# Optimization experiments

Measured on AMD Instinct MI355X. Metric: run time of the kernel, lower is better.

Reference implementation:

```python
import jax, jax.numpy as jnp
import numpy as np

B, D, U = 8192, 2048, 2048  # batch rows, input dim, units
NB_FACTOR = 3
MASK_DENSITY = 1.0 / 16.0  # butterfly-like sparse factor density


def _glorot_uniform(key, shape):
    fan_in, fan_out = shape[0], shape[-1]
    limit = np.sqrt(6.0 / (fan_in + fan_out)).astype(np.float32)
    return jax.random.uniform(key, shape, jnp.float32, -limit, limit)


def setup_inputs() -> dict:
    key = jax.random.key(0)
    kx, km0, km1, km2, kk0, kk1, kk2, ks = jax.random.split(key, 8)
    x = jax.random.normal(kx, (B, D), jnp.float32)
    # Fixed sparsity patterns (constants, like K.constant sparsity_masks)
    m0 = (jax.random.uniform(km0, (D, U)) < MASK_DENSITY).astype(jnp.float32)
    m1 = (jax.random.uniform(km1, (U, U)) < MASK_DENSITY).astype(jnp.float32)
    m2 = (jax.random.uniform(km2, (U, U)) < MASK_DENSITY).astype(jnp.float32)
    k0 = _glorot_uniform(kk0, (D, U))
    k1 = _glorot_uniform(kk1, (U, U))
    k2 = _glorot_uniform(kk2, (U, U))
    scaling = _glorot_uniform(ks, (1,))  # scaler weight, shape (1,)
    bias = jnp.zeros((U,), jnp.float32)
    return {"x": x, "k0": k0, "k1": k1, "k2": k2,
            "m0": m0, "m1": m1, "m2": m2,
            "scaling": scaling, "bias": bias}


def reference(x, k0, k1, k2, m0, m1, m2, scaling, bias):
    # output = activation(scaling * (x @ (k0*m0) @ (k1*m1) @ (k2*m2)) + bias)
    out = x @ (k0 * m0)          # [B, U]
    out = out @ (k1 * m1)        # [B, U]
    out = out @ (k2 * m2)        # [B, U]
    out = scaling * out + bias   # scale then channels-last bias add
    return jax.nn.relu(out)
```

## Files before the change

kernel.cpp:

```cpp
#include <hip/hip_runtime.h>
#include <hip/hip_bf16.h>


typedef __attribute__((ext_vector_type(8))) short  short8;
typedef __attribute__((ext_vector_type(8))) ushort ushort8v;
typedef __attribute__((ext_vector_type(4))) float  f32x4;

#define KD 2048
#define ND 2048

__device__ __forceinline__ ushort f2b(float f) {
    union { float f; unsigned u; } v; v.f = f;
    unsigned r = v.u + 0x7fffu + ((v.u >> 16) & 1u);
    return (ushort)(r >> 16);
}

__device__ __forceinline__ void gload16(const ushort* g, ushort* l) {
    __builtin_amdgcn_global_load_lds(
        (const __attribute__((address_space(1))) void*)g,
        (__attribute__((address_space(3))) void*)l, 16, 0, 0);
}

__global__ __launch_bounds__(256)
void convx(const float* __restrict__ x, ushort* __restrict__ xb)
{
    const size_t i = (size_t)blockIdx.x * 256 + threadIdx.x;
    const float4* src = reinterpret_cast<const float4*>(x) + i * 2;
    const float4 f0 = src[0], f1 = src[1];
    ushort8v u;
    u[0]=f2b(f0.x); u[1]=f2b(f0.y); u[2]=f2b(f0.z); u[3]=f2b(f0.w);
    u[4]=f2b(f1.x); u[5]=f2b(f1.y); u[6]=f2b(f1.z); u[7]=f2b(f1.w);
    reinterpret_cast<ushort8v*>(xb)[i] = u;
}

__global__ __launch_bounds__(256)
void convT3(const float* __restrict__ k0w, const float* __restrict__ k1w,
            const float* __restrict__ k2w, const float* __restrict__ m0w,
            const float* __restrict__ m1w, const float* __restrict__ m2w,
            ushort* __restrict__ wbT)
{
    const int z = blockIdx.z;
    const float* kw = z == 0 ? k0w : (z == 1 ? k1w : k2w);
    const float* mw = z == 0 ? m0w : (z == 1 ? m1w : m2w);
    ushort* o = wbT + (size_t)z * KD * ND;

    __shared__ ushort t[32][36];
    const int tid = threadIdx.x;
    const int bk = blockIdx.x * 32, bn = blockIdx.y * 32;
    {
        const int r = tid >> 3, c = (tid & 7) * 4;
        const size_t g = (size_t)(bk + r) * ND + bn + c;
        const float4 kv = *reinterpret_cast<const float4*>(kw + g);
        const float4 mv = *reinterpret_cast<const float4*>(mw + g);
        t[r][c + 0] = f2b(kv.x * mv.x);
        t[r][c + 1] = f2b(kv.y * mv.y);
        t[r][c + 2] = f2b(kv.z * mv.z);
        t[r][c + 3] = f2b(kv.w * mv.w);
    }
    __syncthreads();
    {
        const int n = tid >> 3, kq = (tid & 7) * 4;
        ushort4 ov;
        ov.x = t[kq + 0][n]; ov.y = t[kq + 1][n];
        ov.z = t[kq + 2][n]; ov.w = t[kq + 3][n];
        *reinterpret_cast<ushort4*>(&o[(size_t)(bn + n) * KD + bk + kq]) = ov;
    }
}

template<int EPI>
__global__ __launch_bounds__(512, 2)
void gemm256(const ushort* __restrict__ A, const ushort* __restrict__ BT,
             void* __restrict__ Cout,
             const float* __restrict__ scaling, const float* __restrict__ bias)
{
    __shared__ ushort S[2][2][2][256 * 32];

    const int tid  = threadIdx.x;
    const int lane = tid & 63;
    const int wid  = tid >> 6;
    const int wr   = wid >> 2, wc = wid & 3;
    const int l15  = lane & 15;
    const int kq   = lane >> 4;
    const int id   = blockIdx.x;
    const int swz  = (id & 7) * 32 + (id >> 3);
    const int bn   = (swz & 7) * 256;
    const int bm   = (swz >> 3) * 256;
    const int srow = lane >> 2;
    const int wrow = wid * 32;
    const int ssw  = ((lane & 3) ^ ((srow >> 1) & 3)) * 8;
    const int rsw  = (kq ^ ((l15 >> 1) & 3)) * 8;

    f32x4 acc[8][4] = {};

#define STAGE(op, bufl, kh, tile, G, g0) do {                                        \
    gload16(G + (size_t)((g0) + wrow + srow)      * KD + (tile)*64 + (kh)*32 + ssw,  \
            &S[bufl][op][kh][(wrow)      * 32]);                                     \
    gload16(G + (size_t)((g0) + wrow + 16 + srow) * KD + (tile)*64 + (kh)*32 + ssw,  \
            &S[bufl][op][kh][(wrow + 16) * 32]);                                     \
  } while (0)

#define BAR()  asm volatile("s_barrier" ::: "memory")
#define VM4()  asm volatile("s_waitcnt vmcnt(4)" ::: "memory")
#define VM0()  asm volatile("s_waitcnt vmcnt(0)" ::: "memory")
#define LGK0() asm volatile("s_waitcnt lgkmcnt(0)" ::: "memory")
#define SB()   __builtin_amdgcn_sched_barrier(0)
#define PRI1() __builtin_amdgcn_s_setprio(1)
#define PRI0() __builtin_amdgcn_s_setprio(0)

#define FA(bufl, kh, m) (*(const short8*)&S[bufl][0][kh][(wr*128 + (m)*16 + l15)*32 + rsw])
#define FB(bufl, kh, n) (*(const short8*)&S[bufl][1][kh][(wc*64  + (n)*16 + l15)*32 + rsw])

#define MF(a_, b_, c_) __builtin_amdgcn_mfma_f32_16x16x32_bf16(a_, b_, c_, 0, 0, 0)

#define MMROW(m, am)                                     \
    acc[m][0] = MF(bf0, am, acc[m][0]);                  \
    acc[m][1] = MF(bf1, am, acc[m][1]);                  \
    acc[m][2] = MF(bf2, am, acc[m][2]);                  \
    acc[m][3] = MF(bf3, am, acc[m][3])

#define PH(bufl, kh, STG, GATE) do {                                                  \
    short8 af0 = FA(bufl,kh,0), af1 = FA(bufl,kh,1), af2 = FA(bufl,kh,2),             \
           af3 = FA(bufl,kh,3), af4 = FA(bufl,kh,4), af5 = FA(bufl,kh,5),             \
           af6 = FA(bufl,kh,6), af7 = FA(bufl,kh,7);                                  \
    short8 bf0 = FB(bufl,kh,0), bf1 = FB(bufl,kh,1),                                  \
           bf2 = FB(bufl,kh,2), bf3 = FB(bufl,kh,3);                                  \
    STG; BAR(); SB(); PRI1();                                                         \
    MMROW(0, af0); MMROW(1, af1); MMROW(2, af2); MMROW(3, af3);                       \
    MMROW(4, af4); MMROW(5, af5); MMROW(6, af6); MMROW(7, af7);                       \
    PRI0(); SB(); LGK0(); GATE; BAR();                                                \
  } while (0)

    STAGE(0, 0, 0, 0, A,  bm); STAGE(1, 0, 0, 0, BT, bn);
    STAGE(0, 0, 1, 0, A,  bm); STAGE(1, 0, 1, 0, BT, bn);
    STAGE(1, 1, 0, 1, BT, bn); STAGE(0, 1, 0, 1, A,  bm);
    VM4();
    BAR();

    const int NITER = KD / 128;
    for (int it = 0; it < NITER - 1; ++it) {
        const int t2 = 2 * it + 2, t3 = 2 * it + 3;
        PH(0, 0, STAGE(1,1,1,t3-2,BT,bn); STAGE(0,1,1,t3-2,A,bm), );
        PH(0, 1, STAGE(1,0,0,t2,BT,bn);   STAGE(0,0,0,t2,A,bm),   VM4());
        PH(1, 0, STAGE(1,0,1,t2,BT,bn);   STAGE(0,0,1,t2,A,bm),   );
        PH(1, 1, STAGE(1,1,0,t3,BT,bn);   STAGE(0,1,0,t3,A,bm),   VM4());
    }
    PH(0, 0, STAGE(1,1,1,31,BT,bn); STAGE(0,1,1,31,A,bm), );
    PH(0, 1, , VM0());
    PH(1, 0, , );
    PH(1, 1, , );

    const float sc = EPI ? scaling[0] : 0.f;
#pragma unroll
    for (int m = 0; m < 8; ++m) {
        const size_t grow = (size_t)(bm + wr * 128 + m * 16 + l15);
#pragma unroll
        for (int n = 0; n < 4; ++n) {
            const int gcol = bn + wc * 64 + n * 16 + kq * 4;
            if constexpr (EPI) {
                const float4 bv = *reinterpret_cast<const float4*>(bias + gcol);
                float4 v;
                v.x = fmaxf(fmaf(sc, acc[m][n][0], bv.x), 0.f);
                v.y = fmaxf(fmaf(sc, acc[m][n][1], bv.y), 0.f);
                v.z = fmaxf(fmaf(sc, acc[m][n][2], bv.z), 0.f);
                v.w = fmaxf(fmaf(sc, acc[m][n][3], bv.w), 0.f);
                *reinterpret_cast<float4*>((float*)Cout + grow * ND + gcol) = v;
            } else {
                ushort4 v;
                v.x = f2b(acc[m][n][0]); v.y = f2b(acc[m][n][1]);
                v.z = f2b(acc[m][n][2]); v.w = f2b(acc[m][n][3]);
                *reinterpret_cast<ushort4*>((ushort*)Cout + grow * ND + gcol) = v;
            }
        }
    }
#undef STAGE
#undef PH
#undef MF
#undef MMROW
#undef FA
#undef FB
}

extern "C" void kernel_launch(void* const* d_in, const int* in_sizes, int n_in,
                              void* d_out, int out_size, void* d_ws, size_t ws_size,
                              hipStream_t stream)
{
    const float* x    = (const float*)d_in[0];
    const float* k0w  = (const float*)d_in[1];
    const float* k1w  = (const float*)d_in[2];
    const float* k2w  = (const float*)d_in[3];
    const float* m0w  = (const float*)d_in[4];
    const float* m1w  = (const float*)d_in[5];
    const float* m2w  = (const float*)d_in[6];
    const float* sc   = (const float*)d_in[7];
    const float* bias = (const float*)d_in[8];

    const int Md = in_sizes[0] / KD;
    const size_t NE = (size_t)Md * KD;

    ushort* act1 = (ushort*)d_out;
    ushort* xb   = (ushort*)d_out + NE;
    float*  out  = (float*)d_out;
    ushort* act2 = (ushort*)d_ws;
    ushort* wbT  = (ushort*)d_ws + NE;

    dim3 bl(256);
    dim3 gX(NE / (256 * 8));
    dim3 gT(KD / 32, ND / 32, 3);
    dim3 gG((ND / 256) * (Md / 256)), bG(512);

    convx <<<gX, bl, 0, stream>>>(x, xb);
    convT3<<<gT, bl, 0, stream>>>(k0w, k1w, k2w, m0w, m1w, m2w, wbT);

    gemm256<0><<<gG, bG, 0, stream>>>(xb,   wbT,                     act1, nullptr, nullptr);
    gemm256<0><<<gG, bG, 0, stream>>>(act1, wbT + (size_t)KD * ND,     act2, nullptr, nullptr);
    gemm256<1><<<gG, bG, 0, stream>>>(act2, wbT + (size_t)2 * KD * ND, out,  sc, bias);
}
```

Baseline: 225.3 us.

## Restructure GEMM main loop to one barrier per K-tile with plain double buffering

Replaces the four-phase-per-iteration pipeline, which used a barrier on each half-tile plus partial vmcnt(4) gating, with a simpler loop. Each 64-wide K tile is one interval: it issues the next tile's loads into the other buffer, runs MFMAs on both K halves, then waits vmcnt(0) and takes a single barrier. The goal is to cut barrier and synchronisation overhead. In exchange the prefetch distance is only one tile and the wait is a full drain, so global-load latency may be exposed more than before.

```diff
diff --git a/kernel.cpp b/kernel.cpp
--- a/kernel.cpp
+++ b/kernel.cpp
@@ -91,6 +91,7 @@
     const int rsw  = (kq ^ ((l15 >> 1) & 3)) * 8;
 
     f32x4 acc[8][4] = {};
+    short8 xa0, xa1, xa2, xa3, xa4, xa5, xa6, xa7, ya0, ya1, ya2, ya3;
 
 #define STAGE(op, bufl, kh, tile, G, g0) do {                                        \
     gload16(G + (size_t)((g0) + wrow + srow)      * KD + (tile)*64 + (kh)*32 + ssw,  \
@@ -100,7 +101,6 @@
   } while (0)
 
 #define BAR()  asm volatile("s_barrier" ::: "memory")
-#define VM4()  asm volatile("s_waitcnt vmcnt(4)" ::: "memory")
 #define VM0()  asm volatile("s_waitcnt vmcnt(0)" ::: "memory")
 #define LGK0() asm volatile("s_waitcnt lgkmcnt(0)" ::: "memory")
 #define SB()   __builtin_amdgcn_sched_barrier(0)
@@ -112,42 +112,50 @@
 
 #define MF(a_, b_, c_) __builtin_amdgcn_mfma_f32_16x16x32_bf16(a_, b_, c_, 0, 0, 0)
 
-#define MMROW(m, am)                                     \
-    acc[m][0] = MF(bf0, am, acc[m][0]);                  \
-    acc[m][1] = MF(bf1, am, acc[m][1]);                  \
-    acc[m][2] = MF(bf2, am, acc[m][2]);                  \
-    acc[m][3] = MF(bf3, am, acc[m][3])
-
-#define PH(bufl, kh, STG, GATE) do {                                                  \
-    short8 af0 = FA(bufl,kh,0), af1 = FA(bufl,kh,1), af2 = FA(bufl,kh,2),             \
-           af3 = FA(bufl,kh,3), af4 = FA(bufl,kh,4), af5 = FA(bufl,kh,5),             \
-           af6 = FA(bufl,kh,6), af7 = FA(bufl,kh,7);                                  \
-    short8 bf0 = FB(bufl,kh,0), bf1 = FB(bufl,kh,1),                                  \
-           bf2 = FB(bufl,kh,2), bf3 = FB(bufl,kh,3);                                  \
-    STG; BAR(); SB(); PRI1();                                                         \
-    MMROW(0, af0); MMROW(1, af1); MMROW(2, af2); MMROW(3, af3);                       \
-    MMROW(4, af4); MMROW(5, af5); MMROW(6, af6); MMROW(7, af7);                       \
-    PRI0(); SB(); LGK0(); GATE; BAR();                                                \
+#define READS(bufl, kh)                                                               \
+    ya0 = FB(bufl,kh,0); ya1 = FB(bufl,kh,1);                                         \
+    ya2 = FB(bufl,kh,2); ya3 = FB(bufl,kh,3);                                         \
+    xa0 = FA(bufl,kh,0); xa1 = FA(bufl,kh,1);                                         \
+    xa2 = FA(bufl,kh,2); xa3 = FA(bufl,kh,3);                                         \
+    xa4 = FA(bufl,kh,4); xa5 = FA(bufl,kh,5);                                         \
+    xa6 = FA(bufl,kh,6); xa7 = FA(bufl,kh,7);
+
+#define MMROW(m, xm)                                                                  \
+    acc[m][0] = MF(ya0, xm, acc[m][0]);                                               \
+    acc[m][1] = MF(ya1, xm, acc[m][1]);                                               \
+    acc[m][2] = MF(ya2, xm, acc[m][2]);                                               \
+    acc[m][3] = MF(ya3, xm, acc[m][3]);
+
+#define MMALL()                                                                       \
+    MMROW(0, xa0) MMROW(1, xa1) MMROW(2, xa2) MMROW(3, xa3)                           \
+    MMROW(4, xa4) MMROW(5, xa5) MMROW(6, xa6) MMROW(7, xa7)
+
+#define INTERVAL(bufl, STG1, STG2, GATE) do {                                         \
+    STG1;                                                                             \
+    READS(bufl, 0);                                                                   \
+    PRI1(); MMALL(); PRI0();                                                          \
+    STG2;                                                                             \
+    READS(bufl, 1);                                                                   \
+    PRI1(); MMALL(); PRI0(); SB();                                                    \
+    LGK0(); GATE; BAR();                                                              \
   } while (0)
 
     STAGE(0, 0, 0, 0, A,  bm); STAGE(1, 0, 0, 0, BT, bn);
     STAGE(0, 0, 1, 0, A,  bm); STAGE(1, 0, 1, 0, BT, bn);
-    STAGE(1, 1, 0, 1, BT, bn); STAGE(0, 1, 0, 1, A,  bm);
-    VM4();
+    VM0();
     BAR();
 
-    const int NITER = KD / 128;
-    for (int it = 0; it < NITER - 1; ++it) {
-        const int t2 = 2 * it + 2, t3 = 2 * it + 3;
-        PH(0, 0, STAGE(1,1,1,t3-2,BT,bn); STAGE(0,1,1,t3-2,A,bm), );
-        PH(0, 1, STAGE(1,0,0,t2,BT,bn);   STAGE(0,0,0,t2,A,bm),   VM4());
-        PH(1, 0, STAGE(1,0,1,t2,BT,bn);   STAGE(0,0,1,t2,A,bm),   );
-        PH(1, 1, STAGE(1,1,0,t3,BT,bn);   STAGE(0,1,0,t3,A,bm),   VM4());
-    }
-    PH(0, 0, STAGE(1,1,1,31,BT,bn); STAGE(0,1,1,31,A,bm), );
-    PH(0, 1, , VM0());
-    PH(1, 0, , );
-    PH(1, 1, , );
+    for (int t = 0; t < 31; ++t) {
+        const int bf = t & 1;
+        INTERVAL(bf,
+                 STAGE(0, bf ^ 1, 0, t + 1, A, bm); STAGE(1, bf ^ 1, 0, t + 1, BT, bn),
+                 STAGE(0, bf ^ 1, 1, t + 1, A, bm); STAGE(1, bf ^ 1, 1, t + 1, BT, bn),
+                 VM0());
+    }
+    READS(1, 0);
+    PRI1(); MMALL(); PRI0();
+    READS(1, 1);
+    PRI1(); MMALL(); PRI0();
 
     const float sc = EPI ? scaling[0] : 0.f;
 #pragma unroll
@@ -173,9 +181,11 @@
         }
     }
 #undef STAGE
-#undef PH
+#undef INTERVAL
 #undef MF
 #undef MMROW
+#undef MMALL
+#undef READS
 #undef FA
 #undef FB
 }
```

Measured after the change: 218.9 us. 2.8% less time.
